# Optimization experiments

Measured on AMD Instinct MI355X. Metric: run time of the kernel, lower is better.

The kernel has to match this reference:

```python
import jax, jax.numpy as jnp
import numpy as np

DIM = 1024
HEADS = 16
HEAD_DIM = DIM // HEADS
SCALE = HEAD_DIM ** -0.5


def setup_inputs() -> dict:
    key = jax.random.key(0)
    ks = jax.random.split(key, 8)
    B, N, C = 2, 2048, DIM
    std = 0.02
    return {
        "x": jax.random.normal(ks[0], (B, N, C), dtype=jnp.float32),
        "e": jax.random.normal(ks[1], (B, N, C), dtype=jnp.float32),
        "W_qkv": jax.random.normal(ks[2], (C, 3 * C), dtype=jnp.float32) * std,
        "W_s": jax.random.normal(ks[3], (C, C), dtype=jnp.float32) * std,
        "W_gate": jax.random.normal(ks[4], (C, C), dtype=jnp.float32) * std,
        "W_proj": jax.random.normal(ks[5], (C, C), dtype=jnp.float32) * std,
        "b_proj": jax.random.normal(ks[6], (C,), dtype=jnp.float32) * std,
    }


def reference(x, e, W_qkv, W_s, W_gate, W_proj, b_proj):
    B, N, C = x.shape
    H, D = HEADS, HEAD_DIM
    # qkv: [B,N,3C] -> [3,B,H,N,D]
    qkv = (x @ W_qkv).reshape(B, N, 3, H, D).transpose(2, 0, 3, 1, 4)
    q, k, v = qkv[0], qkv[1], qkv[2]
    gate = x @ W_gate  # [B,N,C]
    # s bias fused into keys: [B,H,N,D]
    s = (e @ W_s).reshape(B, N, H, D).transpose(0, 2, 1, 3)
    attn = jnp.einsum("bhnd,bhmd->bhnm", q, k + s) * SCALE
    attn = jax.nn.softmax(attn, axis=-1)
    out = jnp.einsum("bhnm,bhmd->bhnd", attn, v)  # [B,H,N,D]
    out = out.transpose(0, 2, 1, 3).reshape(B, N, C)
    out = out * gate
    return out @ W_proj + b_proj
```

## Files before the change

### kernel.cpp

```cpp
#include <hip/hip_runtime.h>
#include <hip/hip_bf16.h>

#define SCALE 0.125f
#define QSCALE 0.18033688f
#define RESCALE_THR 8.0f

typedef __attribute__((ext_vector_type(8))) __bf16 bf16x8;
typedef __attribute__((ext_vector_type(4))) float f32x4;
typedef __attribute__((ext_vector_type(4))) short s16x4;
typedef __hip_bfloat16 bf16;

__device__ __forceinline__ void gl_lds16(const bf16* g, bf16* l) {
  __builtin_amdgcn_global_load_lds(
      (const __attribute__((address_space(1))) void*)g,
      (__attribute__((address_space(3))) void*)l, 16, 0, 0);
}

__device__ __forceinline__ float fexp2(float x) {
#if __has_builtin(__builtin_amdgcn_exp2f)
  return __builtin_amdgcn_exp2f(x);
#else
  return exp2f(x);
#endif
}

__device__ __forceinline__ unsigned cvt_pk_bf16(float lo, float hi) {
  unsigned r;
  asm("v_cvt_pk_bf16_f32 %0, %1, %2" : "=v"(r) : "v"(lo), "v"(hi));
  return r;
}

__device__ __forceinline__ f32x4 zf4() {
  f32x4 v; v[0] = 0.f; v[1] = 0.f; v[2] = 0.f; v[3] = 0.f; return v;
}

__global__ __launch_bounds__(256) void conv2_bf16_k(const float* __restrict__ a,
                                                    const float* __restrict__ b,
                                                    bf16* __restrict__ oa,
                                                    bf16* __restrict__ ob) {
  const int bi = blockIdx.x;
  const float* in = (bi < 4096) ? a : b;
  bf16* out = (bi < 4096) ? oa : ob;
  const int i = ((bi < 4096) ? bi : bi - 4096) * 256 + threadIdx.x;
  const float4 v = reinterpret_cast<const float4*>(in)[i];
  union { bf16 h4[4]; s16x4 s; } u;
  u.h4[0] = __float2bfloat16(v.x);
  u.h4[1] = __float2bfloat16(v.y);
  u.h4[2] = __float2bfloat16(v.z);
  u.h4[3] = __float2bfloat16(v.w);
  reinterpret_cast<s16x4*>(out)[i] = u.s;
}

struct TranspP { const float* s[4]; bf16* d[4]; };
__global__ __launch_bounds__(256) void transp_all_k(TranspP tp) {
  __shared__ float t[32][33];
  const int z = blockIdx.z;
  const int j = (z < 3) ? 0 : z - 2;
  const int coff = (z < 3) ? (z << 10) : 0;
  const int Nsrc = (j == 0) ? 3072 : 1024;
  const float* W = tp.s[j];
  bf16* dst = tp.d[j] + (size_t)((z < 3) ? z : 0) * 1024 * 1024;
  const int tx = threadIdx.x, ty = threadIdx.y;
  const int n0 = blockIdx.x * 32, k0 = blockIdx.y * 32;
#pragma unroll
  for (int i = 0; i < 4; ++i)
    t[ty + 8 * i][tx] = W[(k0 + ty + 8 * i) * Nsrc + coff + n0 + tx];
  __syncthreads();
#pragma unroll
  for (int i = 0; i < 4; ++i)
    dst[(n0 + ty + 8 * i) * 1024 + k0 + tx] = __float2bfloat16(t[tx][ty + 8 * i]);
}

struct GemmP {
  const bf16* A;
  const bf16* B0;
  const bf16* B1;
  const bf16* sT;
  bf16 *q, *k, *vt, *gate, *obf;
  float* out;
  const float* bias;
};

__global__ __launch_bounds__(512, 2) void gemm256_k(GemmP p) {
  constexpr int K = 1024;
  constexpr int NT = 16;
  __shared__ bf16 AB[2][2][256 * 64];
  const int tid = threadIdx.x;
  const int wid = tid >> 6, lane = tid & 63;
  const int l15 = lane & 15, l4 = lane >> 4;
  const int wr = wid >> 2, wc = wid & 3;

  const int bid0 = blockIdx.y * 16 + blockIdx.x;
  const int bid = (bid0 & 7) * 32 + (bid0 >> 3);
  const int m0 = (bid >> 4) * 256, n0 = (bid & 15) * 256;

  const bf16* Arow = p.A + (size_t)m0 * K;
  const bf16* Brow = (n0 >= 3072) ? p.B1 + (size_t)(n0 - 3072) * K
                                  : p.B0 + (size_t)n0 * K;

  f32x4 acc[8][4];
#pragma unroll
  for (int m = 0; m < 8; ++m)
#pragma unroll
    for (int n = 0; n < 4; ++n) acc[m][n] = zf4();

  const int srow = tid >> 3, sc = tid & 7;
  auto stageA = [&](int b, int kt) {
#pragma unroll
    for (int s = 0; s < 4; ++s) {
      const int r = s * 64 + srow;
      const int c2 = sc ^ (r & 7);
      gl_lds16(Arow + (size_t)r * K + kt * 64 + c2 * 8, &AB[b][0][r * 64 + sc * 8]);
    }
  };
  auto stageB = [&](int b, int kt) {
#pragma unroll
    for (int s = 0; s < 4; ++s) {
      const int r = s * 64 + srow;
      const int c2 = sc ^ (r & 7);
      gl_lds16(Brow + (size_t)r * K + kt * 64 + c2 * 8, &AB[b][1][r * 64 + sc * 8]);
    }
  };

  stageA(0, 0);
  stageB(0, 0);
  __syncthreads();
  int cur = 0;

  for (int kt = 0; kt < NT; ++kt) {
    bf16x8 bfv[4][2];
#pragma unroll
    for (int q = 0; q < 4; ++q) {
      bf16x8 af[2][2];
#pragma unroll
      for (int mm = 0; mm < 2; ++mm) {
        const int row = wr * 128 + (q * 2 + mm) * 16 + l15;
#pragma unroll
        for (int ks = 0; ks < 2; ++ks)
          af[mm][ks] = *reinterpret_cast<const bf16x8*>(
              &AB[cur][0][row * 64 + ((ks * 4 + l4) ^ (row & 7)) * 8]);
      }
      if (q == 0) {
#pragma unroll
        for (int n = 0; n < 4; ++n) {
          const int row = wc * 64 + n * 16 + l15;
#pragma unroll
          for (int ks = 0; ks < 2; ++ks)
            bfv[n][ks] = *reinterpret_cast<const bf16x8*>(
                &AB[cur][1][row * 64 + ((ks * 4 + l4) ^ (row & 7)) * 8]);
        }
      }
      if (q == 0 && kt + 1 < NT) stageA(cur ^ 1, kt + 1);
      if (q == 1 && kt + 1 < NT) stageB(cur ^ 1, kt + 1);

      __builtin_amdgcn_s_barrier();
      __builtin_amdgcn_s_setprio(1);
#pragma unroll
      for (int mm = 0; mm < 2; ++mm)
#pragma unroll
        for (int n = 0; n < 4; ++n)
#pragma unroll
          for (int ks = 0; ks < 2; ++ks)
            acc[q * 2 + mm][n] = __builtin_amdgcn_mfma_f32_16x16x32_bf16(
                af[mm][ks], bfv[n][ks], acc[q * 2 + mm][n], 0, 0, 0);
      __builtin_amdgcn_s_setprio(0);
      __builtin_amdgcn_s_barrier();
    }
    asm volatile("s_waitcnt vmcnt(0)" ::: "memory");
    __builtin_amdgcn_s_barrier();
    cur ^= 1;
  }

#pragma unroll
  for (int m = 0; m < 8; ++m) {
    const int gr0 = m0 + wr * 128 + m * 16 + l4 * 4;
    const int bb = gr0 >> 11;
    const int nn0 = gr0 & 2047;
#pragma unroll
    for (int n = 0; n < 4; ++n) {
      const int gc = n0 + wc * 64 + n * 16 + l15;
      if (gc < 3072) {
        const int t = gc >> 10, hd = gc & 1023;
        const int h = hd >> 6, d = hd & 63;
        const int base = ((bb * 16 + h) * 2048 + nn0) * 64 + d;
        if (t == 0) {
#pragma unroll
          for (int r = 0; r < 4; ++r)
            p.q[base + r * 64] = __float2bfloat16(acc[m][n][r] * QSCALE);
        } else if (t == 1) {
#pragma unroll
          for (int r = 0; r < 4; ++r)
            p.k[base + r * 64] =
                __float2bfloat16(acc[m][n][r] + __bfloat162float(p.sT[base + r * 64]));
        } else {
          union { bf16 h4[4]; s16x4 s; } u;
#pragma unroll
          for (int r = 0; r < 4; ++r) u.h4[r] = __float2bfloat16(acc[m][n][r]);
          *reinterpret_cast<s16x4*>(&p.vt[((bb * 16 + h) * 64 + d) * 2048 + nn0]) = u.s;
        }
      } else {
        const int gcc = gc - 3072;
#pragma unroll
        for (int r = 0; r < 4; ++r)
          p.gate[(gr0 + r) * 1024 + gcc] = __float2bfloat16(acc[m][n][r]);
      }
    }
  }
}

template <int EPI>
__global__ __launch_bounds__(256) void gemm2_k(GemmP p) {
  constexpr int K = 1024;
  __shared__ bf16 As[64 * 32];
  __shared__ bf16 Bs[128 * 32];
  const int tid = threadIdx.x;
  const int wid = tid >> 6, lane = tid & 63;
  const int l15 = lane & 15, l4 = lane >> 4;
  const int wc = wid;
  const int m0 = blockIdx.y * 64, n0 = blockIdx.x * 128;
  const bf16* Arow = p.A + m0 * K;
  const bf16* Brow = p.B0 + n0 * K;

  f32x4 acc[4][2];
#pragma unroll
  for (int m = 0; m < 4; ++m)
#pragma unroll
    for (int n = 0; n < 2; ++n) acc[m][n] = zf4();

  const int srowA = tid >> 2, skc = tid & 3;
  for (int kt = 0; kt < K; kt += 32) {
    gl_lds16(Arow + srowA * K + kt + skc * 8, As + wid * 512);
#pragma unroll
    for (int it = 0; it < 2; ++it)
      gl_lds16(Brow + (it * 64 + srowA) * K + kt + skc * 8, Bs + it * 2048 + wid * 512);
    __syncthreads();
    bf16x8 af[4], bfr[2];
#pragma unroll
    for (int m = 0; m < 4; ++m)
      af[m] = *reinterpret_cast<const bf16x8*>(&As[(m * 16 + l15) * 32 + 8 * l4]);
#pragma unroll
    for (int n = 0; n < 2; ++n)
      bfr[n] = *reinterpret_cast<const bf16x8*>(&Bs[(wc * 32 + n * 16 + l15) * 32 + 8 * l4]);
#pragma unroll
    for (int m = 0; m < 4; ++m)
#pragma unroll
      for (int n = 0; n < 2; ++n)
        acc[m][n] = __builtin_amdgcn_mfma_f32_16x16x32_bf16(af[m], bfr[n], acc[m][n], 0, 0, 0);
    __syncthreads();
  }

#pragma unroll
  for (int m = 0; m < 4; ++m) {
    const int gr0 = m0 + m * 16 + l4 * 4;
    const int bb = gr0 >> 11;
    const int nn0 = gr0 & 2047;
#pragma unroll
    for (int n = 0; n < 2; ++n) {
      const int gc = n0 + wc * 32 + n * 16 + l15;
      if (EPI == 0) {
        const int h = gc >> 6, d = gc & 63;
        bf16* dst = p.obf + ((bb * 16 + h) * 2048 + nn0) * 64 + d;
#pragma unroll
        for (int r = 0; r < 4; ++r) dst[r * 64] = __float2bfloat16(acc[m][n][r]);
      } else {
        const float bias = p.bias[gc];
#pragma unroll
        for (int r = 0; r < 4; ++r) p.out[(gr0 + r) * 1024 + gc] = acc[m][n][r] + bias;
      }
    }
  }
}

__global__ __launch_bounds__(256) void flash_k(const bf16* __restrict__ qT,
                                               const bf16* __restrict__ kTb,
                                               const bf16* __restrict__ vTt,
                                               const bf16* __restrict__ gateb,
                                               bf16* __restrict__ attng) {
  __shared__ bf16 Ks[2][64 * 64];
  __shared__ bf16 Vs[2][64 * 64];
  const int tid = threadIdx.x;
  const int wid = tid >> 6, lane = tid & 63;
  const int l15 = lane & 15, l4 = lane >> 4;
  const int hbit = lane >> 5;
  const int qt = blockIdx.x, bh = blockIdx.y;
  const int qr0 = qt * 128 + wid * 32;
  const bf16* qbase = qT + (bh * 2048 + qr0) * 64;
  bf16x8 qf[2][2];
#pragma unroll
  for (int g = 0; g < 2; ++g)
#pragma unroll
    for (int kk = 0; kk < 2; ++kk)
      qf[g][kk] = *reinterpret_cast<const bf16x8*>(
          &qbase[(g * 16 + l15) * 64 + kk * 32 + 8 * l4]);
  const bf16* kbase = kTb + bh * 2048 * 64;
  const bf16* vbase = vTt + bh * 64 * 2048;
  const int srcQ0 = (((lane & 16) << 1) | (lane & 15)) << 2;
  const int srcQ1 = srcQ0 | 64;

  f32x4 o[2][4];
#pragma unroll
  for (int g = 0; g < 2; ++g)
#pragma unroll
    for (int i = 0; i < 4; ++i) o[g][i] = zf4();
  float mrun[2] = {-1e30f, -1e30f}, lrun[2] = {0.f, 0.f};
  const int srow = tid >> 3, sc = tid & 7;

  auto stage = [&](int b, int kt) {
#pragma unroll
    for (int it = 0; it < 2; ++it) {
      const int row = it * 32 + srow;
      const int c2 = sc ^ (row & 7);
      gl_lds16(kbase + (kt * 64 + row) * 64 + c2 * 8, &Ks[b][it * 2048 + wid * 512]);
      gl_lds16(vbase + row * 2048 + kt * 64 + c2 * 8, &Vs[b][it * 2048 + wid * 512]);
    }
  };

  stage(0, 0);
  __syncthreads();
  int cur = 0;

  for (int kt = 0; kt < 32; ++kt) {
    if (kt < 31) stage(cur ^ 1, kt + 1);

    f32x4 sa[2][4];
#pragma unroll
    for (int g = 0; g < 2; ++g)
#pragma unroll
      for (int n = 0; n < 4; ++n) sa[g][n] = zf4();
    __builtin_amdgcn_s_setprio(1);
#pragma unroll
    for (int kk = 0; kk < 2; ++kk) {
#pragma unroll
      for (int n = 0; n < 4; ++n) {
        const int key = n * 16 + l15;
        const bf16x8 kv = *reinterpret_cast<const bf16x8*>(
            &Ks[cur][key * 64 + ((kk * 4 + l4) ^ (key & 7)) * 8]);
#pragma unroll
        for (int g = 0; g < 2; ++g)
          sa[g][n] = __builtin_amdgcn_mfma_f32_16x16x32_bf16(kv, qf[g][kk], sa[g][n], 0, 0, 0);
      }
    }
    __builtin_amdgcn_s_setprio(0);

    float mt[2];
#pragma unroll
    for (int g = 0; g < 2; ++g) {
      float m = sa[g][0][0];
#pragma unroll
      for (int n = 0; n < 4; ++n)
#pragma unroll
        for (int r = 0; r < 4; ++r) m = fmaxf(m, sa[g][n][r]);
      m = fmaxf(m, __shfl_xor(m, 16, 64));
      mt[g] = fmaxf(m, __shfl_xor(m, 32, 64));
    }

    const int okg = (mt[0] <= mrun[0] + RESCALE_THR) & (mt[1] <= mrun[1] + RESCALE_THR);
    const bool upd = !__all(okg);
    float fac[2] = {1.f, 1.f};
    if (upd) {
#pragma unroll
      for (int g = 0; g < 2; ++g) {
        const float mn = fmaxf(mrun[g], mt[g]);
        fac[g] = fexp2(mrun[g] - mn);
        mrun[g] = mn;
      }
    }

    int Cp[2][4][2];
#pragma unroll
    for (int g = 0; g < 2; ++g) {
      float psum = 0.f;
      float p[4][4];
#pragma unroll
      for (int n = 0; n < 4; ++n)
#pragma unroll
        for (int r = 0; r < 4; ++r) {
          p[n][r] = fexp2(sa[g][n][r] - mrun[g]);
          psum += p[n][r];
        }
      psum += __shfl_xor(psum, 16, 64);
      psum += __shfl_xor(psum, 32, 64);
      if (upd) {
        lrun[g] = lrun[g] * fac[g] + psum;
#pragma unroll
        for (int nd = 0; nd < 4; ++nd)
#pragma unroll
          for (int r = 0; r < 4; ++r) o[g][nd][r] *= fac[g];
      } else {
        lrun[g] += psum;
      }
#pragma unroll
      for (int n = 0; n < 4; ++n) {
        Cp[g][n][0] = (int)cvt_pk_bf16(p[n][0], p[n][1]);
        Cp[g][n][1] = (int)cvt_pk_bf16(p[n][2], p[n][3]);
      }
    }

    __builtin_amdgcn_s_setprio(1);
#pragma unroll
    for (int kk = 0; kk < 2; ++kk) {
      bf16x8 pw[2];
#pragma unroll
      for (int g = 0; g < 2; ++g) {
        const int x0 = __builtin_amdgcn_ds_bpermute(srcQ0, Cp[g][2 * kk][0]);
        const int x1 = __builtin_amdgcn_ds_bpermute(srcQ0, Cp[g][2 * kk + 1][0]);
        const int y0 = __builtin_amdgcn_ds_bpermute(srcQ0, Cp[g][2 * kk][1]);
        const int y1 = __builtin_amdgcn_ds_bpermute(srcQ0, Cp[g][2 * kk + 1][1]);
        const int z0 = __builtin_amdgcn_ds_bpermute(srcQ1, Cp[g][2 * kk][0]);
        const int z1 = __builtin_amdgcn_ds_bpermute(srcQ1, Cp[g][2 * kk + 1][0]);
        const int t0 = __builtin_amdgcn_ds_bpermute(srcQ1, Cp[g][2 * kk][1]);
        const int t1 = __builtin_amdgcn_ds_bpermute(srcQ1, Cp[g][2 * kk + 1][1]);
        union { int u[4]; bf16x8 v; } u;
        u.u[0] = hbit ? x1 : x0;
        u.u[1] = hbit ? y1 : y0;
        u.u[2] = hbit ? z1 : z0;
        u.u[3] = hbit ? t1 : t0;
        pw[g] = u.v;
      }
#pragma unroll
      for (int nd = 0; nd < 4; ++nd) {
        const int d = nd * 16 + l15;
        const bf16x8 vv = *reinterpret_cast<const bf16x8*>(
            &Vs[cur][d * 64 + ((kk * 4 + l4) ^ (d & 7)) * 8]);
#pragma unroll
        for (int g = 0; g < 2; ++g)
          o[g][nd] = __builtin_amdgcn_mfma_f32_16x16x32_bf16(vv, pw[g], o[g][nd], 0, 0, 0);
      }
    }
    __builtin_amdgcn_s_setprio(0);

    __syncthreads();
    cur ^= 1;
  }

  const int bb = bh >> 4, h = bh & 15;
#pragma unroll
  for (int g = 0; g < 2; ++g) {
    const int grow = bb * 2048 + qr0 + g * 16 + l15;
    const float inv = 1.0f / lrun[g];
#pragma unroll
    for (int nd = 0; nd < 4; ++nd) {
      const int gi = grow * 1024 + h * 64 + nd * 16 + l4 * 4;
      union { s16x4 s; bf16 h4[4]; } gu, ou;
      gu.s = *reinterpret_cast<const s16x4*>(&gateb[gi]);
#pragma unroll
      for (int r = 0; r < 4; ++r)
        ou.h4[r] = __float2bfloat16(o[g][nd][r] * inv * __bfloat162float(gu.h4[r]));
      *reinterpret_cast<s16x4*>(&attng[gi]) = ou.s;
    }
  }
}

extern "C" void kernel_launch(void* const* d_in, const int* in_sizes, int n_in,
                              void* d_out, int out_size, void* d_ws, size_t ws_size,
                              hipStream_t stream) {
  const float* x = (const float*)d_in[0];
  const float* e = (const float*)d_in[1];
  const float* Wqkv = (const float*)d_in[2];
  const float* Ws = (const float*)d_in[3];
  const float* Wgate = (const float*)d_in[4];
  const float* Wproj = (const float*)d_in[5];
  const float* bproj = (const float*)d_in[6];
  float* out = (float*)d_out;

  char* w = (char*)d_ws;
  auto carve = [&](size_t bytes) -> void* {
    void* p = (void*)w;
    w += (bytes + 255) & ~size_t(255);
    return p;
  };
  bf16* xbf    = (bf16*)carve(4096UL * 1024 * 2);
  bf16* ebf    = (bf16*)carve(4096UL * 1024 * 2);
  bf16* Wqkvt  = (bf16*)carve(3072UL * 1024 * 2);
  bf16* Wst    = (bf16*)carve(1024UL * 1024 * 2);
  bf16* Wgatet = (bf16*)carve(1024UL * 1024 * 2);
  bf16* Wprojt = (bf16*)carve(1024UL * 1024 * 2);
  bf16* kTb    = (bf16*)carve(32UL * 2048 * 64 * 2);
  bf16* vTt    = (bf16*)carve(32UL * 64 * 2048 * 2);
  bf16* sT     = (bf16*)carve(32UL * 2048 * 64 * 2);
  bf16* gateb  = (bf16*)carve(4096UL * 1024 * 2);
  bf16* qT     = ebf;
  bf16* attng  = sT;

  conv2_bf16_k<<<8192, 256, 0, stream>>>(x, e, xbf, ebf);

  TranspP tp{};
  tp.s[0] = Wqkv; tp.s[1] = Ws; tp.s[2] = Wgate; tp.s[3] = Wproj;
  tp.d[0] = Wqkvt; tp.d[1] = Wst; tp.d[2] = Wgatet; tp.d[3] = Wprojt;
  transp_all_k<<<dim3(32, 32, 6), dim3(32, 8), 0, stream>>>(tp);

  GemmP ps{};
  ps.A = ebf; ps.B0 = Wst; ps.obf = sT;
  gemm2_k<0><<<dim3(8, 64), 256, 0, stream>>>(ps);

  GemmP pq{};
  pq.A = xbf; pq.B0 = Wqkvt; pq.B1 = Wgatet; pq.sT = sT;
  pq.q = qT; pq.k = kTb; pq.vt = vTt; pq.gate = gateb;
  gemm256_k<<<dim3(16, 16), 512, 0, stream>>>(pq);

  flash_k<<<dim3(16, 32), 256, 0, stream>>>(qT, kTb, vTt, gateb, attng);

  GemmP pp{};
  pp.A = attng; pp.B0 = Wprojt; pp.out = out; pp.bias = bproj;
  gemm2_k<2><<<dim3(8, 64), 256, 0, stream>>>(pp);
}
```

Measured before the change: 268.7 us.

## Double-buffer swizzled 128x64 GEMM tiles and merge prep kernels

```diff
diff --git a/kernel.cpp b/kernel.cpp
--- a/kernel.cpp
+++ b/kernel.cpp
@@ -34,33 +34,34 @@
   f32x4 v; v[0] = 0.f; v[1] = 0.f; v[2] = 0.f; v[3] = 0.f; return v;
 }
 
-__global__ __launch_bounds__(256) void conv2_bf16_k(const float* __restrict__ a,
-                                                    const float* __restrict__ b,
-                                                    bf16* __restrict__ oa,
-                                                    bf16* __restrict__ ob) {
-  const int bi = blockIdx.x;
-  const float* in = (bi < 4096) ? a : b;
-  bf16* out = (bi < 4096) ? oa : ob;
-  const int i = ((bi < 4096) ? bi : bi - 4096) * 256 + threadIdx.x;
-  const float4 v = reinterpret_cast<const float4*>(in)[i];
-  union { bf16 h4[4]; s16x4 s; } u;
-  u.h4[0] = __float2bfloat16(v.x);
-  u.h4[1] = __float2bfloat16(v.y);
-  u.h4[2] = __float2bfloat16(v.z);
-  u.h4[3] = __float2bfloat16(v.w);
-  reinterpret_cast<s16x4*>(out)[i] = u.s;
-}
-
-struct TranspP { const float* s[4]; bf16* d[4]; };
-__global__ __launch_bounds__(256) void transp_all_k(TranspP tp) {
+struct PrepP { const float* s[4]; bf16* d[4]; const float *x, *e; bf16 *xb, *eb; };
+__global__ __launch_bounds__(256) void prep_k(PrepP tp) {
+  const int tid = threadIdx.x;
+  const int z = blockIdx.z;
+  if (z == 6) {
+    const int i = (blockIdx.y * 32 + blockIdx.x) * 256 + tid;
+#pragma unroll
+    for (int u = 0; u < 8; ++u) {
+      const int idx = u * 262144 + i;
+      const bool isx = idx < 1048576;
+      const int k = isx ? idx : idx - 1048576;
+      const float4 v = reinterpret_cast<const float4*>(isx ? tp.x : tp.e)[k];
+      union { bf16 h4[4]; s16x4 s; } u4;
+      u4.h4[0] = __float2bfloat16(v.x);
+      u4.h4[1] = __float2bfloat16(v.y);
+      u4.h4[2] = __float2bfloat16(v.z);
+      u4.h4[3] = __float2bfloat16(v.w);
+      reinterpret_cast<s16x4*>(isx ? tp.xb : tp.eb)[k] = u4.s;
+    }
+    return;
+  }
   __shared__ float t[32][33];
-  const int z = blockIdx.z;
   const int j = (z < 3) ? 0 : z - 2;
   const int coff = (z < 3) ? (z << 10) : 0;
   const int Nsrc = (j == 0) ? 3072 : 1024;
   const float* W = tp.s[j];
   bf16* dst = tp.d[j] + (size_t)((z < 3) ? z : 0) * 1024 * 1024;
-  const int tx = threadIdx.x, ty = threadIdx.y;
+  const int tx = tid & 31, ty = tid >> 5;
   const int n0 = blockIdx.x * 32, k0 = blockIdx.y * 32;
 #pragma unroll
   for (int i = 0; i < 4; ++i)
@@ -209,17 +210,21 @@
 }
 
 template <int EPI>
-__global__ __launch_bounds__(256) void gemm2_k(GemmP p) {
+__global__ __launch_bounds__(256) void gemm128_k(GemmP p) {
   constexpr int K = 1024;
-  __shared__ bf16 As[64 * 32];
-  __shared__ bf16 Bs[128 * 32];
+  constexpr int NT = 16;
+  __shared__ bf16 AB[2][128 * 64 + 64 * 64];
   const int tid = threadIdx.x;
   const int wid = tid >> 6, lane = tid & 63;
   const int l15 = lane & 15, l4 = lane >> 4;
-  const int wc = wid;
-  const int m0 = blockIdx.y * 64, n0 = blockIdx.x * 128;
-  const bf16* Arow = p.A + m0 * K;
-  const bf16* Brow = p.B0 + n0 * K;
+  const int wr = wid >> 1, wc = wid & 1;
+
+  const int bid0 = blockIdx.y * 16 + blockIdx.x;
+  const int bid = (bid0 & 7) * 64 + (bid0 >> 3);
+  const int m0 = (bid >> 4) * 128, n0 = (bid & 15) * 64;
+
+  const bf16* Arow = p.A + (size_t)m0 * K;
+  const bf16* Brow = p.B0 + (size_t)n0 * K;
 
   f32x4 acc[4][2];
 #pragma unroll
@@ -227,31 +232,76 @@
 #pragma unroll
     for (int n = 0; n < 2; ++n) acc[m][n] = zf4();
 
-  const int srowA = tid >> 2, skc = tid & 3;
-  for (int kt = 0; kt < K; kt += 32) {
-    gl_lds16(Arow + srowA * K + kt + skc * 8, As + wid * 512);
-#pragma unroll
-    for (int it = 0; it < 2; ++it)
-      gl_lds16(Brow + (it * 64 + srowA) * K + kt + skc * 8, Bs + it * 2048 + wid * 512);
-    __syncthreads();
-    bf16x8 af[4], bfr[2];
-#pragma unroll
-    for (int m = 0; m < 4; ++m)
-      af[m] = *reinterpret_cast<const bf16x8*>(&As[(m * 16 + l15) * 32 + 8 * l4]);
-#pragma unroll
-    for (int n = 0; n < 2; ++n)
-      bfr[n] = *reinterpret_cast<const bf16x8*>(&Bs[(wc * 32 + n * 16 + l15) * 32 + 8 * l4]);
-#pragma unroll
-    for (int m = 0; m < 4; ++m)
-#pragma unroll
-      for (int n = 0; n < 2; ++n)
-        acc[m][n] = __builtin_amdgcn_mfma_f32_16x16x32_bf16(af[m], bfr[n], acc[m][n], 0, 0, 0);
-    __syncthreads();
+  const int srow = tid >> 3, sc = tid & 7;
+  auto stageA = [&](int b, int kt) {
+#pragma unroll
+    for (int s = 0; s < 4; ++s) {
+      const int r = s * 32 + srow;
+      const int c2 = sc ^ (r & 7);
+      gl_lds16(Arow + (size_t)r * K + kt * 64 + c2 * 8, &AB[b][r * 64 + sc * 8]);
+    }
+  };
+  auto stageB = [&](int b, int kt) {
+#pragma unroll
+    for (int s = 0; s < 2; ++s) {
+      const int r = s * 32 + srow;
+      const int c2 = sc ^ (r & 7);
+      gl_lds16(Brow + (size_t)r * K + kt * 64 + c2 * 8, &AB[b][8192 + r * 64 + sc * 8]);
+    }
+  };
+
+  stageA(0, 0);
+  stageB(0, 0);
+  __syncthreads();
+  int cur = 0;
+
+  for (int kt = 0; kt < NT; ++kt) {
+    bf16x8 bfv[2][2];
+#pragma unroll
+    for (int q = 0; q < 2; ++q) {
+      bf16x8 af[2][2];
+#pragma unroll
+      for (int mm = 0; mm < 2; ++mm) {
+        const int row = wr * 64 + (q * 2 + mm) * 16 + l15;
+#pragma unroll
+        for (int ks = 0; ks < 2; ++ks)
+          af[mm][ks] = *reinterpret_cast<const bf16x8*>(
+              &AB[cur][row * 64 + ((ks * 4 + l4) ^ (row & 7)) * 8]);
+      }
+      if (q == 0) {
+#pragma unroll
+        for (int n = 0; n < 2; ++n) {
+          const int row = wc * 32 + n * 16 + l15;
+#pragma unroll
+          for (int ks = 0; ks < 2; ++ks)
+            bfv[n][ks] = *reinterpret_cast<const bf16x8*>(
+                &AB[cur][8192 + row * 64 + ((ks * 4 + l4) ^ (row & 7)) * 8]);
+        }
+      }
+      if (q == 0 && kt + 1 < NT) stageA(cur ^ 1, kt + 1);
+      if (q == 1 && kt + 1 < NT) stageB(cur ^ 1, kt + 1);
+
+      __builtin_amdgcn_s_barrier();
+      __builtin_amdgcn_s_setprio(1);
+#pragma unroll
+      for (int mm = 0; mm < 2; ++mm)
+#pragma unroll
+        for (int n = 0; n < 2; ++n)
+#pragma unroll
+          for (int ks = 0; ks < 2; ++ks)
+            acc[q * 2 + mm][n] = __builtin_amdgcn_mfma_f32_16x16x32_bf16(
+                af[mm][ks], bfv[n][ks], acc[q * 2 + mm][n], 0, 0, 0);
+      __builtin_amdgcn_s_setprio(0);
+      __builtin_amdgcn_s_barrier();
+    }
+    asm volatile("s_waitcnt vmcnt(0)" ::: "memory");
+    __builtin_amdgcn_s_barrier();
+    cur ^= 1;
   }
 
 #pragma unroll
   for (int m = 0; m < 4; ++m) {
-    const int gr0 = m0 + m * 16 + l4 * 4;
+    const int gr0 = m0 + wr * 64 + m * 16 + l4 * 4;
     const int bb = gr0 >> 11;
     const int nn0 = gr0 & 2047;
 #pragma unroll
@@ -482,16 +532,15 @@
   bf16* qT     = ebf;
   bf16* attng  = sT;
 
-  conv2_bf16_k<<<8192, 256, 0, stream>>>(x, e, xbf, ebf);
-
-  TranspP tp{};
+  PrepP tp{};
   tp.s[0] = Wqkv; tp.s[1] = Ws; tp.s[2] = Wgate; tp.s[3] = Wproj;
   tp.d[0] = Wqkvt; tp.d[1] = Wst; tp.d[2] = Wgatet; tp.d[3] = Wprojt;
-  transp_all_k<<<dim3(32, 32, 6), dim3(32, 8), 0, stream>>>(tp);
+  tp.x = x; tp.e = e; tp.xb = xbf; tp.eb = ebf;
+  prep_k<<<dim3(32, 32, 7), 256, 0, stream>>>(tp);
 
   GemmP ps{};
   ps.A = ebf; ps.B0 = Wst; ps.obf = sT;
-  gemm2_k<0><<<dim3(8, 64), 256, 0, stream>>>(ps);
+  gemm128_k<0><<<dim3(16, 32), 256, 0, stream>>>(ps);
 
   GemmP pq{};
   pq.A = xbf; pq.B0 = Wqkvt; pq.B1 = Wgatet; pq.sT = sT;
@@ -502,5 +551,5 @@
 
   GemmP pp{};
   pp.A = attng; pp.B0 = Wprojt; pp.out = out; pp.bias = bproj;
-  gemm2_k<2><<<dim3(8, 64), 256, 0, stream>>>(pp);
-}
+  gemm128_k<1><<<dim3(16, 32), 256, 0, stream>>>(pp);
+}
```

Result: no change. 267.9 us (-0.3%).
